# Performance work log

Hardware: AMD Instinct MI355X
Metric: run time of the kernel (lower is better)

The kernel has to match this reference:

```python
import jax, jax.numpy as jnp
import numpy as np

N_NODES = 100000
N_EDGES = 1600000
N_GRAPHS = 512
BN_EPS = 1e-5


def setup_inputs() -> dict:
    key = jax.random.key(0)
    ks = jax.random.split(key, 16)
    x = jax.random.normal(ks[0], (N_NODES, 66), dtype=jnp.float32)
    edge_index = jax.random.randint(ks[1], (2, N_EDGES), 0, N_NODES, dtype=jnp.int64)
    edge_attr = jax.random.normal(ks[2], (N_EDGES, 1), dtype=jnp.float32)
    batch = jnp.sort(jax.random.randint(ks[3], (N_NODES,), 0, N_GRAPHS, dtype=jnp.int64))
    def glorot(k, shape):
        lim = np.sqrt(6.0 / (shape[0] + shape[1]))
        return jax.random.uniform(k, shape, jnp.float32, -lim, lim)
    return {
        "x": x, "edge_index": edge_index, "edge_attr": edge_attr, "batch": batch,
        "W1": glorot(ks[4], (66, 64)), "b1": jnp.zeros((64,), jnp.float32),
        "g1": jnp.ones((64,), jnp.float32), "be1": jnp.zeros((64,), jnp.float32),
        "W2": glorot(ks[5], (64, 32)), "b2": jnp.zeros((32,), jnp.float32),
        "g2": jnp.ones((32,), jnp.float32), "be2": jnp.zeros((32,), jnp.float32),
        "Wm1": glorot(ks[6], (64, 32)), "bm1": jnp.zeros((32,), jnp.float32),
        "Wm2": glorot(ks[7], (32, 2)), "bm2": jnp.zeros((2,), jnp.float32),
    }


def gcn_conv(x, W, b, src, dst, n_nodes):
    # PyG GCNConv: add self-loops, symmetric D^-1/2 (A+I) D^-1/2 normalization.
    xw = x @ W                                             # [N, F]
    deg = jnp.zeros((n_nodes,), xw.dtype).at[dst].add(1.0) + 1.0  # incl. self-loop
    dinv = jax.lax.rsqrt(deg)                              # deg^-1/2
    coef = dinv[src] * dinv[dst]                           # [E]
    agg = jnp.zeros_like(xw).at[dst].add(xw[src] * coef[:, None])
    agg = agg + xw * (dinv * dinv)[:, None]                # self-loop messages
    return agg + b


def batch_norm(x, gamma, beta):
    # training-mode BN over the node dimension (reference is deterministic)
    mu = jnp.mean(x, axis=0)
    var = jnp.mean(jnp.square(x - mu), axis=0)
    return gamma * (x - mu) * jax.lax.rsqrt(var + BN_EPS) + beta


def reference(x, edge_index, edge_attr, batch,
              W1, b1, g1, be1, W2, b2, g2, be2, Wm1, bm1, Wm2, bm2):
    src, dst = edge_index[0], edge_index[1]
    h = x[:, :66]
    h = jax.nn.elu(batch_norm(gcn_conv(h, W1, b1, src, dst, N_NODES), g1, be1))
    # dropout omitted (eval-mode reference)
    h = jax.nn.elu(batch_norm(gcn_conv(h, W2, b2, src, dst, N_NODES), g2, be2))
    counts = jax.ops.segment_sum(jnp.ones((N_NODES,), h.dtype), batch, num_segments=N_GRAPHS)
    mean_pool = jax.ops.segment_sum(h, batch, num_segments=N_GRAPHS) / jnp.maximum(counts, 1.0)[:, None]
    max_pool = jax.ops.segment_max(h, batch, num_segments=N_GRAPHS)
    max_pool = jnp.where(counts[:, None] > 0, max_pool, 0.0)
    g = jnp.concatenate([mean_pool, max_pool], axis=1)     # [G, 64]
    g = jax.nn.elu(g @ Wm1 + bm1)
    return g @ Wm2 + bm2                                   # [G, num_classes]
```

## Files before the change

### kernel.cpp

```cpp
#include <hip/hip_runtime.h>
#include <math.h>

constexpr int NN = 100000;
constexpr int NE = 1600000;
constexpr int NG = 512;
constexpr int NBKT = (NN + 127) / 128;
constexpr int BSTR = 2560;
constexpr int PADREG = BSTR + 896;
constexpr int BCAP = 3072;
constexpr int NHALF = 50048;

typedef unsigned short bf16_t;
typedef unsigned int u32x4 __attribute__((ext_vector_type(4)));
__device__ __forceinline__ bf16_t f2bf(float f) {
    unsigned u = __float_as_uint(f);
    unsigned r = (u + 0x7fffu + ((u >> 16) & 1u)) >> 16;
    return (bf16_t)r;
}
__device__ __forceinline__ float bflo(unsigned u) { return __uint_as_float(u << 16); }
__device__ __forceinline__ float bfhi(unsigned u) { return __uint_as_float(u & 0xffff0000u); }
__device__ __forceinline__ unsigned bfpack(float lo, float hi) {
    return ((unsigned)f2bf(hi) << 16) | (unsigned)f2bf(lo);
}
__device__ __forceinline__ float eluf(float x) {
    return x > 0.f ? x : expm1f(x);
}

__global__ __launch_bounds__(1024) void k_scatter_bkt(const int* __restrict__ src,
                                                      const int* __restrict__ dst,
                                                      int* __restrict__ bktCur,
                                                      int* __restrict__ ebuf) {
    __shared__ int cnt[NBKT];
    __shared__ int base[NBKT];
    int tid = threadIdx.x;
    for (int i = tid; i < NBKT; i += 1024) cnt[i] = 0;
    __syncthreads();
    int per = (NE + gridDim.x - 1) / gridDim.x;
    int e0 = blockIdx.x * per;
    int e1 = min(e0 + per, NE);
    for (int e = e0 + tid; e < e1; e += 1024) {
        int d = __builtin_nontemporal_load(dst + e);
        atomicAdd(&cnt[d >> 7], 1);
    }
    __syncthreads();
    for (int i = tid; i < NBKT; i += 1024) {
        int c = cnt[i];
        base[i] = i * BSTR + (c ? atomicAdd(&bktCur[i], c) : 0);
        cnt[i] = 0;
    }
    __syncthreads();
    for (int e = e0 + tid; e < e1; e += 1024) {
        int s = __builtin_nontemporal_load(src + e);
        int d = __builtin_nontemporal_load(dst + e);
        int b = d >> 7;
        int off = atomicAdd(&cnt[b], 1);
        ebuf[base[b] + off] = (s << 7) | (d & 127);
    }
}

__global__ __launch_bounds__(256) void k_bktsort(const int* __restrict__ bktCur,
                                                 const int* __restrict__ ebuf,
                                                 int* __restrict__ csr,
                                                 int2* __restrict__ rowInfo,
                                                 float* __restrict__ dinv,
                                                 const int* __restrict__ batch,
                                                 int* __restrict__ gptr) {
    int b = blockIdx.x, tid = threadIdx.x;
    if (b == NBKT) {
        for (int g = tid; g <= NG; g += 256) {
            if (g == NG) { gptr[NG] = NN; continue; }
            int lo = 0, hi = NN;
            while (lo < hi) {
                int mid = (lo + hi) >> 1;
                if (batch[mid] < g) lo = mid + 1; else hi = mid;
            }
            gptr[g] = lo;
        }
        return;
    }
    __shared__ int sbuf[BCAP];
    __shared__ int cnt[128], scn[128], cur[128];
    __shared__ int padTotS;
    int base = b * BSTR;
    int n = min(bktCur[b], BSTR);
    int pbase = b * PADREG;
    for (int i = tid; i < n; i += 256) sbuf[i] = __builtin_nontemporal_load(ebuf + base + i);
    if (tid < 128) cnt[tid] = 0;
    __syncthreads();
    for (int i = tid; i < n; i += 256) atomicAdd(&cnt[sbuf[i] & 127], 1);
    __syncthreads();
    int deg = (tid < 128) ? cnt[tid] : 0;
    int pcnt = (deg + 7) & ~7;
    if (tid < 128) scn[tid] = pcnt;
    __syncthreads();
    for (int off = 1; off < 128; off <<= 1) {
        int t = (tid < 128 && tid >= off) ? scn[tid - off] : 0;
        __syncthreads();
        if (tid < 128) scn[tid] += t;
        __syncthreads();
    }
    if (tid == 127) padTotS = scn[127];
    if (tid < 128) {
        int ex = scn[tid] - pcnt;
        cur[tid] = ex;
        int node = b * 128 + tid;
        if (node < NN) {
            rowInfo[node] = make_int2(pbase + ex, pbase + ex + pcnt);
            dinv[node] = rsqrtf((float)deg + 1.0f);
        }
    }
    __syncthreads();
    int padTot = padTotS;
    for (int i = tid; i < padTot; i += 256) csr[pbase + i] = NN;
    __syncthreads();
    for (int i = tid; i < n; i += 256) {
        int p = sbuf[i];
        int pos = atomicAdd(&cur[p & 127], 1);
        csr[pbase + pos] = p >> 7;
    }
}

__global__ void k_gemm1(const float* __restrict__ x, const float* __restrict__ W1,
                        const float* __restrict__ dinv, bf16_t* __restrict__ y1b) {
    __shared__ __align__(16) float sx[64 * 68];
    __shared__ __align__(16) float sw[66 * 64];
    int tid = threadIdx.x;
    for (int i = tid; i < 66 * 32; i += 256) ((float2*)sw)[i] = ((const float2*)W1)[i];
    int base = blockIdx.x * 64;
    int rows = min(64, NN - base);
    int cnt2v = rows * 33;
    const float2* xp = (const float2*)(x + base * 66);
    for (int i = tid; i < cnt2v; i += 256) {
        int r = i / 33, kk = i - r * 33;
        ((float2*)(sx + r * 68))[kk] = xp[i];
    }
    __syncthreads();
    int tr = tid >> 4, tc = tid & 15;
    const float* sxr = sx + tr * 4 * 68;
    const float* swc = sw + tc * 4;
    float acc[4][4];
#pragma unroll
    for (int r = 0; r < 4; ++r)
#pragma unroll
        for (int c = 0; c < 4; ++c) acc[r][c] = 0.f;
#pragma unroll 4
    for (int ks = 0; ks < 64; ks += 4) {
        float4 a0 = *(const float4*)(sxr + 0 * 68 + ks);
        float4 a1 = *(const float4*)(sxr + 1 * 68 + ks);
        float4 a2 = *(const float4*)(sxr + 2 * 68 + ks);
        float4 a3 = *(const float4*)(sxr + 3 * 68 + ks);
        float4 b0 = *(const float4*)(swc + (ks + 0) * 64);
        float4 b1 = *(const float4*)(swc + (ks + 1) * 64);
        float4 b2 = *(const float4*)(swc + (ks + 2) * 64);
        float4 b3 = *(const float4*)(swc + (ks + 3) * 64);
#define FMA4(ar, bv, kk) do { \
        acc[0][0] = fmaf(a0.ar, bv.x, acc[0][0]); acc[0][1] = fmaf(a0.ar, bv.y, acc[0][1]); \
        acc[0][2] = fmaf(a0.ar, bv.z, acc[0][2]); acc[0][3] = fmaf(a0.ar, bv.w, acc[0][3]); \
        acc[1][0] = fmaf(a1.ar, bv.x, acc[1][0]); acc[1][1] = fmaf(a1.ar, bv.y, acc[1][1]); \
        acc[1][2] = fmaf(a1.ar, bv.z, acc[1][2]); acc[1][3] = fmaf(a1.ar, bv.w, acc[1][3]); \
        acc[2][0] = fmaf(a2.ar, bv.x, acc[2][0]); acc[2][1] = fmaf(a2.ar, bv.y, acc[2][1]); \
        acc[2][2] = fmaf(a2.ar, bv.z, acc[2][2]); acc[2][3] = fmaf(a2.ar, bv.w, acc[2][3]); \
        acc[3][0] = fmaf(a3.ar, bv.x, acc[3][0]); acc[3][1] = fmaf(a3.ar, bv.y, acc[3][1]); \
        acc[3][2] = fmaf(a3.ar, bv.z, acc[3][2]); acc[3][3] = fmaf(a3.ar, bv.w, acc[3][3]); } while (0)
        FMA4(x, b0, 0); FMA4(y, b1, 1); FMA4(z, b2, 2); FMA4(w, b3, 3);
#undef FMA4
    }
#pragma unroll
    for (int k = 64; k < 66; ++k) {
        float4 bt = *(const float4*)(swc + k * 64);
#pragma unroll
        for (int r = 0; r < 4; ++r) {
            float av = sxr[r * 68 + k];
            acc[r][0] = fmaf(av, bt.x, acc[r][0]);
            acc[r][1] = fmaf(av, bt.y, acc[r][1]);
            acc[r][2] = fmaf(av, bt.z, acc[r][2]);
            acc[r][3] = fmaf(av, bt.w, acc[r][3]);
        }
    }
    bf16_t* dstp = y1b + (tc >> 2) * ((NN + 1) * 16) + (tc & 3) * 4;
#pragma unroll
    for (int r = 0; r < 4; ++r) {
        int nn = base + tr * 4 + r;
        if (nn < NN) {
            float di = dinv[nn];
            ushort4 o;
            o.x = f2bf(di * acc[r][0]); o.y = f2bf(di * acc[r][1]);
            o.z = f2bf(di * acc[r][2]); o.w = f2bf(di * acc[r][3]);
            *(ushort4*)(dstp + (size_t)nn * 16) = o;
        } else if (nn == NN) {
            ushort4 o; o.x = 0; o.y = 0; o.z = 0; o.w = 0;
            *(ushort4*)(dstp + (size_t)nn * 16) = o;
        }
    }
}

template<int NSL>
__global__ __launch_bounds__(256) void k_gather(const int2* __restrict__ rowInfo,
                                                const int* __restrict__ csr,
                                                const float* __restrict__ dinv,
                                                const uint4* __restrict__ yb,
                                                uint4* __restrict__ aggb,
                                                float* __restrict__ sums,
                                                float* __restrict__ sqs,
                                                int n0, int n1) {
    constexpr int SH = (NSL == 4) ? 2 : 1;
    __shared__ float sSum[16], sSq[16];
    int tid = threadIdx.x;
    if (tid < 16) { sSum[tid] = 0.f; sSq[tid] = 0.f; }
    __syncthreads();
    int slice = blockIdx.x & (NSL - 1);
    int part = blockIdx.x >> SH;
    int nparts = gridDim.x >> SH;
    int lane = tid & 1;
    int grp = tid >> 1;
    const uint4* y = yb + (size_t)slice * ((NN + 1) * 2) + lane;
    uint4* agg = aggb + (size_t)slice * (NN * 2) + lane;
    float s[8], q[8];
#pragma unroll
    for (int k = 0; k < 8; ++k) { s[k] = 0.f; q[k] = 0.f; }
    for (int n = n0 + part * 128 + grp; n < n1; n += nparts * 128) {
        int2 ri = rowInfo[n];
        float a[8];
#pragma unroll
        for (int k = 0; k < 8; ++k) a[k] = 0.f;
        int j = ri.x;
        unsigned long long c0 = 0, c1 = 0, c2 = 0, c3 = 0;
        if (j < ri.y) {
            const unsigned long long* cp = (const unsigned long long*)(csr + j);
            c0 = cp[0]; c1 = cp[1]; c2 = cp[2]; c3 = cp[3];
        }
        while (j < ri.y) {
            int i0 = (int)(c0 & 0xffffffffu), i1 = (int)(c0 >> 32);
            int i2 = (int)(c1 & 0xffffffffu), i3 = (int)(c1 >> 32);
            int i4 = (int)(c2 & 0xffffffffu), i5 = (int)(c2 >> 32);
            int i6 = (int)(c3 & 0xffffffffu), i7 = (int)(c3 >> 32);
            j += 8;
            uint4 v0 = y[i0 * 2];
            uint4 v1 = y[i1 * 2];
            uint4 v2 = y[i2 * 2];
            uint4 v3 = y[i3 * 2];
            uint4 v4 = y[i4 * 2];
            uint4 v5 = y[i5 * 2];
            uint4 v6 = y[i6 * 2];
            uint4 v7 = y[i7 * 2];
            if (j < ri.y) {
                const unsigned long long* np = (const unsigned long long*)(csr + j);
                c0 = np[0]; c1 = np[1]; c2 = np[2]; c3 = np[3];
            }
#define ACC8(v) do { \
            a[0] += bflo((v).x); a[1] += bfhi((v).x); \
            a[2] += bflo((v).y); a[3] += bfhi((v).y); \
            a[4] += bflo((v).z); a[5] += bfhi((v).z); \
            a[6] += bflo((v).w); a[7] += bfhi((v).w); } while (0)
            ACC8(v0); ACC8(v1); ACC8(v2); ACC8(v3);
            ACC8(v4); ACC8(v5); ACC8(v6); ACC8(v7);
#undef ACC8
        }
        uint4 vs = y[n * 2];
        float di = dinv[n];
        a[0] = di * (a[0] + bflo(vs.x)); a[1] = di * (a[1] + bfhi(vs.x));
        a[2] = di * (a[2] + bflo(vs.y)); a[3] = di * (a[3] + bfhi(vs.y));
        a[4] = di * (a[4] + bflo(vs.z)); a[5] = di * (a[5] + bfhi(vs.z));
        a[6] = di * (a[6] + bflo(vs.w)); a[7] = di * (a[7] + bfhi(vs.w));
        u32x4 o;
        o.x = bfpack(a[0], a[1]); o.y = bfpack(a[2], a[3]);
        o.z = bfpack(a[4], a[5]); o.w = bfpack(a[6], a[7]);
        __builtin_nontemporal_store(o, (u32x4*)(agg + n * 2));
#pragma unroll
        for (int k = 0; k < 8; ++k) {
            float av = (k == 0) ? a[0] : (k == 1) ? a[1] : (k == 2) ? a[2] : (k == 3) ? a[3]
                     : (k == 4) ? a[4] : (k == 5) ? a[5] : (k == 6) ? a[6] : a[7];
            s[k] += av; q[k] += av * av;
        }
    }
#pragma unroll
    for (int k = 0; k < 8; ++k) {
        float sv = s[k], qv = q[k];
#pragma unroll
        for (int off = 2; off < 64; off <<= 1) {
            sv += __shfl_xor(sv, off);
            qv += __shfl_xor(qv, off);
        }
        if ((tid & 63) < 2) {
            atomicAdd(&sSum[lane * 8 + k], sv);
            atomicAdd(&sSq[lane * 8 + k], qv);
        }
    }
    __syncthreads();
    if (tid < 16) {
        unsafeAtomicAdd(&sums[slice * 16 + tid], sSum[tid]);
        unsafeAtomicAdd(&sqs[slice * 16 + tid], sSq[tid]);
    }
}

__global__ void k_bn_gemm2(const unsigned* __restrict__ agg1b, const float* __restrict__ sums,
                           const float* __restrict__ sqs, const float* __restrict__ gamma,
                           const float* __restrict__ beta, const float* __restrict__ W2,
                           const float* __restrict__ dinv, bf16_t* __restrict__ y2b) {
    constexpr int RB = 32;
    __shared__ __align__(16) float sh[RB * 64];
    __shared__ __align__(16) float sWt[32 * 68];
    __shared__ float sscale[64], sshift[64];
    int tid = threadIdx.x;
    if (tid < 64) {
        float mu = sums[tid] * (1.0f / NN);
        float var = sqs[tid] * (1.0f / NN) - mu * mu;
        float sc = gamma[tid] * rsqrtf(var + 1e-5f);
        sscale[tid] = sc;
        sshift[tid] = beta[tid] - mu * sc;
    }
#pragma unroll
    for (int i = tid; i < 64 * 32; i += 256) {
        int k = i >> 5, c = i & 31;
        sWt[c * 68 + k] = W2[i];
    }
    __syncthreads();
    int base = blockIdx.x * RB;
#pragma unroll
    for (int rr = 0; rr < RB / 8; ++rr) {
        int r = (tid >> 5) + rr * 8, qq = tid & 31;
        int slice = qq >> 3, lane = qq & 7;
        int n = base + r;
        int col = slice * 16 + lane * 2;
        float v0 = 0.f, v1 = 0.f;
        if (n < NN) {
            unsigned u = agg1b[(size_t)slice * NN * 8 + (size_t)n * 8 + lane];
            v0 = eluf(fmaf(bflo(u), sscale[col], sshift[col]));
            v1 = eluf(fmaf(bfhi(u), sscale[col + 1], sshift[col + 1]));
        }
        sh[r * 64 + col] = v0;
        sh[r * 64 + col + 1] = v1;
    }
    __syncthreads();
    int c = tid & 31;
    bf16_t* dstp = y2b + (c >> 4) * ((NN + 1) * 16) + (c & 15);
    const float* swr = sWt + c * 68;
#pragma unroll
    for (int rr = 0; rr < RB / 8; ++rr) {
        int r = (tid >> 5) + rr * 8;
        int n = base + r;
        if (n < NN) {
            const float* shr = sh + r * 64;
            float acc = 0.f;
#pragma unroll
            for (int k4 = 0; k4 < 64; k4 += 4) {
                float4 av = *(const float4*)(shr + k4);
                float4 bv = *(const float4*)(swr + k4);
                acc = fmaf(av.x, bv.x, acc);
                acc = fmaf(av.y, bv.y, acc);
                acc = fmaf(av.z, bv.z, acc);
                acc = fmaf(av.w, bv.w, acc);
            }
            dstp[(size_t)n * 16] = f2bf(dinv[n] * acc);
        } else if (n == NN) {
            dstp[(size_t)NN * 16] = 0;
        }
    }
}

__global__ void k_poolmlp(const unsigned* __restrict__ agg2b, const float* __restrict__ sums,
                          const float* __restrict__ sqs, const float* __restrict__ gamma,
                          const float* __restrict__ beta, const int* __restrict__ gptr,
                          const float* __restrict__ Wm1, const float* __restrict__ bm1,
                          const float* __restrict__ Wm2, const float* __restrict__ bm2,
                          float* __restrict__ out) {
    __shared__ float sscale[32], sshift[32];
    __shared__ float red[256];
    __shared__ float gr[64];
    __shared__ float h[32];
    int tid = threadIdx.x;
    if (tid < 32) {
        float mu = sums[tid] * (1.0f / NN);
        float var = sqs[tid] * (1.0f / NN) - mu * mu;
        float sc = gamma[tid] * rsqrtf(var + 1e-5f);
        sscale[tid] = sc;
        sshift[tid] = beta[tid] - mu * sc;
    }
    __syncthreads();
    int g = blockIdx.x;
    int c = tid & 31, r = tid >> 5;
    int beg = gptr[g], end = gptr[g + 1];
    float scl = sscale[c], shf = sshift[c];
    const unsigned* ap = agg2b + (size_t)(c >> 4) * NN * 8 + ((c >> 1) & 7);
    bool hi = (c & 1);
    float s = 0.f, m = -INFINITY;
    for (int n = beg + r; n < end; n += 8) {
        unsigned u = ap[n * 8];
        float v = eluf(fmaf(hi ? bfhi(u) : bflo(u), scl, shf));
        s += v;
        m = fmaxf(m, v);
    }
    red[tid] = s;
    __syncthreads();
    int cnt = end - beg;
    if (r == 0) {
        float stot = 0.f;
#pragma unroll
        for (int i = 0; i < 8; ++i) stot += red[i * 32 + c];
        gr[c] = stot / fmaxf((float)cnt, 1.f);
    }
    __syncthreads();
    red[tid] = m;
    __syncthreads();
    if (r == 0) {
        float mtot = -INFINITY;
#pragma unroll
        for (int i = 0; i < 8; ++i) mtot = fmaxf(mtot, red[i * 32 + c]);
        gr[32 + c] = (cnt > 0) ? mtot : 0.f;
    }
    __syncthreads();
    if (tid < 32) {
        float acc = bm1[tid];
#pragma unroll
        for (int k = 0; k < 64; ++k) acc = fmaf(gr[k], Wm1[k * 32 + tid], acc);
        h[tid] = eluf(acc);
    }
    __syncthreads();
    if (tid < 2) {
        float acc = bm2[tid];
#pragma unroll
        for (int k = 0; k < 32; ++k) acc = fmaf(h[k], Wm2[k * 2 + tid], acc);
        out[g * 2 + tid] = acc;
    }
}

extern "C" void kernel_launch(void* const* d_in, const int* in_sizes, int n_in,
                              void* d_out, int out_size, void* d_ws, size_t ws_size,
                              hipStream_t stream) {
    const float* x    = (const float*)d_in[0];
    const int*   eidx = (const int*)d_in[1];
    const int*   src  = eidx;
    const int*   dst  = eidx + NE;
    const int*   batch = (const int*)d_in[3];
    const float* W1  = (const float*)d_in[4];
    const float* g1  = (const float*)d_in[6];
    const float* be1 = (const float*)d_in[7];
    const float* W2  = (const float*)d_in[8];
    const float* g2  = (const float*)d_in[10];
    const float* be2 = (const float*)d_in[11];
    const float* Wm1 = (const float*)d_in[12];
    const float* bm1 = (const float*)d_in[13];
    const float* Wm2 = (const float*)d_in[14];
    const float* bm2 = (const float*)d_in[15];
    float* out = (float*)d_out;

    constexpr int CSRSZ = NBKT * PADREG + 16;
    int*    bktCur  = (int*)d_ws;
    float*  S       = (float*)(bktCur + 800);
    int*    gptr    = (int*)(S + 512);
    int*    csr     = gptr + 544;
    int2*   rowInfo = (int2*)(csr + CSRSZ);
    float*  dinv    = (float*)(rowInfo + 100000);
    bf16_t* y1b     = (bf16_t*)(dinv + 100000);
    bf16_t* agg1b   = y1b + (NN + 1) * 64;
    bf16_t* y2b     = agg1b + NN * 64;
    bf16_t* agg2b   = y2b + (NN + 1) * 32;
    int*    ebuf    = (int*)y2b;

    float* sum1 = S;        float* sq1 = S + 64;
    float* sum2 = S + 128;  float* sq2 = S + 160;

    (void)hipMemsetAsync(bktCur, 0, (800 + 512) * sizeof(int), stream);

    k_scatter_bkt<<<512, 1024, 0, stream>>>(src, dst, bktCur, ebuf);
    k_bktsort<<<NBKT + 1, 256, 0, stream>>>(bktCur, ebuf, csr, rowInfo, dinv, batch, gptr);

    k_gemm1<<<(NN + 63) / 64, 256, 0, stream>>>(x, W1, dinv, y1b);
    k_gather<4><<<1564, 256, 0, stream>>>(rowInfo, csr, dinv,
                                          (const uint4*)y1b, (uint4*)agg1b,
                                          sum1, sq1, 0, NHALF);
    k_gather<4><<<1564, 256, 0, stream>>>(rowInfo, csr, dinv,
                                          (const uint4*)y1b, (uint4*)agg1b,
                                          sum1, sq1, NHALF, NN);

    k_bn_gemm2<<<NN / 32 + 1, 256, 0, stream>>>((const unsigned*)agg1b, sum1, sq1,
                                                g1, be1, W2, dinv, y2b);
    k_gather<2><<<782, 256, 0, stream>>>(rowInfo, csr, dinv,
                                         (const uint4*)y2b, (uint4*)agg2b,
                                         sum2, sq2, 0, NHALF);
    k_gather<2><<<782, 256, 0, stream>>>(rowInfo, csr, dinv,
                                         (const uint4*)y2b, (uint4*)agg2b,
                                         sum2, sq2, NHALF, NN);

    k_poolmlp<<<NG, 256, 0, stream>>>((const unsigned*)agg2b, sum2, sq2, g2, be2, gptr,
                                      Wm1, bm1, Wm2, bm2, out);
}
```

Baseline: 304.1 us.

## Fuse bucket sort with first GEMM and merge split gather launches

Merges the bucket-sort kernel and the first GEMM into one launch. GEMM blocks compute node degrees locally from the bucketed edge buffer instead of waiting for dinv from the sort kernel. The two half-range gather launches per layer are also merged into single launches with doubled grids. This removes launch gaps and the sort-to-GEMM dependency, at the cost of GEMM blocks rescanning each bucket's edges (twice per bucket) and larger shared memory per block.

New measurement: 280.9 us. -7.6%, faster.

```diff
diff --git a/kernel.cpp b/kernel.cpp
--- a/kernel.cpp
+++ b/kernel.cpp
@@ -8,7 +8,7 @@
 constexpr int BSTR = 2560;
 constexpr int PADREG = BSTR + 896;
 constexpr int BCAP = 3072;
-constexpr int NHALF = 50048;
+constexpr int NT1 = (NN + 63) / 64;
 
 typedef unsigned short bf16_t;
 typedef unsigned int u32x4 __attribute__((ext_vector_type(4)));
@@ -58,14 +58,101 @@
     }
 }
 
-__global__ __launch_bounds__(256) void k_bktsort(const int* __restrict__ bktCur,
-                                                 const int* __restrict__ ebuf,
-                                                 int* __restrict__ csr,
-                                                 int2* __restrict__ rowInfo,
-                                                 float* __restrict__ dinv,
-                                                 const int* __restrict__ batch,
-                                                 int* __restrict__ gptr) {
-    int b = blockIdx.x, tid = threadIdx.x;
+__global__ __launch_bounds__(256) void k_sort_gemm1(const int* __restrict__ bktCur,
+                                                    const int* __restrict__ ebuf,
+                                                    int* __restrict__ csr,
+                                                    int2* __restrict__ rowInfo,
+                                                    float* __restrict__ dinv,
+                                                    const int* __restrict__ batch,
+                                                    int* __restrict__ gptr,
+                                                    const float* __restrict__ x,
+                                                    const float* __restrict__ W1,
+                                                    bf16_t* __restrict__ y1b) {
+    __shared__ __align__(16) unsigned smem_u[8640];
+    int tid = threadIdx.x;
+    if (blockIdx.x < NT1) {
+        float* sx = (float*)smem_u;
+        float* sw = sx + 64 * 68;
+        int*  deg = (int*)(sw + 66 * 64);
+        if (tid < 64) deg[tid] = 0;
+        for (int i = tid; i < 66 * 32; i += 256) ((float2*)sw)[i] = ((const float2*)W1)[i];
+        int base = blockIdx.x * 64;
+        int rows = min(64, NN - base);
+        int cnt2v = rows * 33;
+        const float2* xp = (const float2*)(x + base * 66);
+        for (int i = tid; i < cnt2v; i += 256) {
+            int r = i / 33, kk = i - r * 33;
+            ((float2*)(sx + r * 68))[kk] = xp[i];
+        }
+        int bkt = base >> 7;
+        int half = (base >> 6) & 1;
+        int ne = min(bktCur[bkt], BSTR);
+        for (int i = tid; i < ne; i += 256) {
+            int e = ebuf[bkt * BSTR + i];
+            int d = e & 127;
+            if ((d >> 6) == half) atomicAdd(&deg[d & 63], 1);
+        }
+        __syncthreads();
+        int tr = tid >> 4, tc = tid & 15;
+        const float* sxr = sx + tr * 4 * 68;
+        const float* swc = sw + tc * 4;
+        float acc[4][4];
+#pragma unroll
+        for (int r = 0; r < 4; ++r)
+#pragma unroll
+            for (int c = 0; c < 4; ++c) acc[r][c] = 0.f;
+#pragma unroll 4
+        for (int ks = 0; ks < 64; ks += 4) {
+            float4 a0 = *(const float4*)(sxr + 0 * 68 + ks);
+            float4 a1 = *(const float4*)(sxr + 1 * 68 + ks);
+            float4 a2 = *(const float4*)(sxr + 2 * 68 + ks);
+            float4 a3 = *(const float4*)(sxr + 3 * 68 + ks);
+            float4 b0 = *(const float4*)(swc + (ks + 0) * 64);
+            float4 b1 = *(const float4*)(swc + (ks + 1) * 64);
+            float4 b2 = *(const float4*)(swc + (ks + 2) * 64);
+            float4 b3 = *(const float4*)(swc + (ks + 3) * 64);
+#define FMA4(ar, bv) do { \
+            acc[0][0] = fmaf(a0.ar, bv.x, acc[0][0]); acc[0][1] = fmaf(a0.ar, bv.y, acc[0][1]); \
+            acc[0][2] = fmaf(a0.ar, bv.z, acc[0][2]); acc[0][3] = fmaf(a0.ar, bv.w, acc[0][3]); \
+            acc[1][0] = fmaf(a1.ar, bv.x, acc[1][0]); acc[1][1] = fmaf(a1.ar, bv.y, acc[1][1]); \
+            acc[1][2] = fmaf(a1.ar, bv.z, acc[1][2]); acc[1][3] = fmaf(a1.ar, bv.w, acc[1][3]); \
+            acc[2][0] = fmaf(a2.ar, bv.x, acc[2][0]); acc[2][1] = fmaf(a2.ar, bv.y, acc[2][1]); \
+            acc[2][2] = fmaf(a2.ar, bv.z, acc[2][2]); acc[2][3] = fmaf(a2.ar, bv.w, acc[2][3]); \
+            acc[3][0] = fmaf(a3.ar, bv.x, acc[3][0]); acc[3][1] = fmaf(a3.ar, bv.y, acc[3][1]); \
+            acc[3][2] = fmaf(a3.ar, bv.z, acc[3][2]); acc[3][3] = fmaf(a3.ar, bv.w, acc[3][3]); } while (0)
+            FMA4(x, b0); FMA4(y, b1); FMA4(z, b2); FMA4(w, b3);
+#undef FMA4
+        }
+#pragma unroll
+        for (int k = 64; k < 66; ++k) {
+            float4 bt = *(const float4*)(swc + k * 64);
+#pragma unroll
+            for (int r = 0; r < 4; ++r) {
+                float av = sxr[r * 68 + k];
+                acc[r][0] = fmaf(av, bt.x, acc[r][0]);
+                acc[r][1] = fmaf(av, bt.y, acc[r][1]);
+                acc[r][2] = fmaf(av, bt.z, acc[r][2]);
+                acc[r][3] = fmaf(av, bt.w, acc[r][3]);
+            }
+        }
+        bf16_t* dstp = y1b + (tc >> 2) * ((NN + 1) * 16) + (tc & 3) * 4;
+#pragma unroll
+        for (int r = 0; r < 4; ++r) {
+            int nn = base + tr * 4 + r;
+            if (nn < NN) {
+                float di = rsqrtf((float)deg[tr * 4 + r] + 1.0f);
+                ushort4 o;
+                o.x = f2bf(di * acc[r][0]); o.y = f2bf(di * acc[r][1]);
+                o.z = f2bf(di * acc[r][2]); o.w = f2bf(di * acc[r][3]);
+                *(ushort4*)(dstp + (size_t)nn * 16) = o;
+            } else if (nn == NN) {
+                ushort4 o; o.x = 0; o.y = 0; o.z = 0; o.w = 0;
+                *(ushort4*)(dstp + (size_t)nn * 16) = o;
+            }
+        }
+        return;
+    }
+    int b = blockIdx.x - NT1;
     if (b == NBKT) {
         for (int g = tid; g <= NG; g += 256) {
             if (g == NG) { gptr[NG] = NN; continue; }
@@ -78,9 +165,11 @@
         }
         return;
     }
-    __shared__ int sbuf[BCAP];
-    __shared__ int cnt[128], scn[128], cur[128];
-    __shared__ int padTotS;
+    int* sbuf = (int*)smem_u;
+    int* cnt  = sbuf + BCAP;
+    int* scn  = cnt + 128;
+    int* cur  = scn + 128;
+    int* padTotS = cur + 128;
     int base = b * BSTR;
     int n = min(bktCur[b], BSTR);
     int pbase = b * PADREG;
@@ -99,7 +188,7 @@
         if (tid < 128) scn[tid] += t;
         __syncthreads();
     }
-    if (tid == 127) padTotS = scn[127];
+    if (tid == 127) *padTotS = scn[127];
     if (tid < 128) {
         int ex = scn[tid] - pcnt;
         cur[tid] = ex;
@@ -110,87 +199,13 @@
         }
     }
     __syncthreads();
-    int padTot = padTotS;
+    int padTot = *padTotS;
     for (int i = tid; i < padTot; i += 256) csr[pbase + i] = NN;
     __syncthreads();
     for (int i = tid; i < n; i += 256) {
         int p = sbuf[i];
         int pos = atomicAdd(&cur[p & 127], 1);
         csr[pbase + pos] = p >> 7;
-    }
-}
-
-__global__ void k_gemm1(const float* __restrict__ x, const float* __restrict__ W1,
-                        const float* __restrict__ dinv, bf16_t* __restrict__ y1b) {
-    __shared__ __align__(16) float sx[64 * 68];
-    __shared__ __align__(16) float sw[66 * 64];
-    int tid = threadIdx.x;
-    for (int i = tid; i < 66 * 32; i += 256) ((float2*)sw)[i] = ((const float2*)W1)[i];
-    int base = blockIdx.x * 64;
-    int rows = min(64, NN - base);
-    int cnt2v = rows * 33;
-    const float2* xp = (const float2*)(x + base * 66);
-    for (int i = tid; i < cnt2v; i += 256) {
-        int r = i / 33, kk = i - r * 33;
-        ((float2*)(sx + r * 68))[kk] = xp[i];
-    }
-    __syncthreads();
-    int tr = tid >> 4, tc = tid & 15;
-    const float* sxr = sx + tr * 4 * 68;
-    const float* swc = sw + tc * 4;
-    float acc[4][4];
-#pragma unroll
-    for (int r = 0; r < 4; ++r)
-#pragma unroll
-        for (int c = 0; c < 4; ++c) acc[r][c] = 0.f;
-#pragma unroll 4
-    for (int ks = 0; ks < 64; ks += 4) {
-        float4 a0 = *(const float4*)(sxr + 0 * 68 + ks);
-        float4 a1 = *(const float4*)(sxr + 1 * 68 + ks);
-        float4 a2 = *(const float4*)(sxr + 2 * 68 + ks);
-        float4 a3 = *(const float4*)(sxr + 3 * 68 + ks);
-        float4 b0 = *(const float4*)(swc + (ks + 0) * 64);
-        float4 b1 = *(const float4*)(swc + (ks + 1) * 64);
-        float4 b2 = *(const float4*)(swc + (ks + 2) * 64);
-        float4 b3 = *(const float4*)(swc + (ks + 3) * 64);
-#define FMA4(ar, bv, kk) do { \
-        acc[0][0] = fmaf(a0.ar, bv.x, acc[0][0]); acc[0][1] = fmaf(a0.ar, bv.y, acc[0][1]); \
-        acc[0][2] = fmaf(a0.ar, bv.z, acc[0][2]); acc[0][3] = fmaf(a0.ar, bv.w, acc[0][3]); \
-        acc[1][0] = fmaf(a1.ar, bv.x, acc[1][0]); acc[1][1] = fmaf(a1.ar, bv.y, acc[1][1]); \
-        acc[1][2] = fmaf(a1.ar, bv.z, acc[1][2]); acc[1][3] = fmaf(a1.ar, bv.w, acc[1][3]); \
-        acc[2][0] = fmaf(a2.ar, bv.x, acc[2][0]); acc[2][1] = fmaf(a2.ar, bv.y, acc[2][1]); \
-        acc[2][2] = fmaf(a2.ar, bv.z, acc[2][2]); acc[2][3] = fmaf(a2.ar, bv.w, acc[2][3]); \
-        acc[3][0] = fmaf(a3.ar, bv.x, acc[3][0]); acc[3][1] = fmaf(a3.ar, bv.y, acc[3][1]); \
-        acc[3][2] = fmaf(a3.ar, bv.z, acc[3][2]); acc[3][3] = fmaf(a3.ar, bv.w, acc[3][3]); } while (0)
-        FMA4(x, b0, 0); FMA4(y, b1, 1); FMA4(z, b2, 2); FMA4(w, b3, 3);
-#undef FMA4
-    }
-#pragma unroll
-    for (int k = 64; k < 66; ++k) {
-        float4 bt = *(const float4*)(swc + k * 64);
-#pragma unroll
-        for (int r = 0; r < 4; ++r) {
-            float av = sxr[r * 68 + k];
-            acc[r][0] = fmaf(av, bt.x, acc[r][0]);
-            acc[r][1] = fmaf(av, bt.y, acc[r][1]);
-            acc[r][2] = fmaf(av, bt.z, acc[r][2]);
-            acc[r][3] = fmaf(av, bt.w, acc[r][3]);
-        }
-    }
-    bf16_t* dstp = y1b + (tc >> 2) * ((NN + 1) * 16) + (tc & 3) * 4;
-#pragma unroll
-    for (int r = 0; r < 4; ++r) {
-        int nn = base + tr * 4 + r;
-        if (nn < NN) {
-            float di = dinv[nn];
-            ushort4 o;
-            o.x = f2bf(di * acc[r][0]); o.y = f2bf(di * acc[r][1]);
-            o.z = f2bf(di * acc[r][2]); o.w = f2bf(di * acc[r][3]);
-            *(ushort4*)(dstp + (size_t)nn * 16) = o;
-        } else if (nn == NN) {
-            ushort4 o; o.x = 0; o.y = 0; o.z = 0; o.w = 0;
-            *(ushort4*)(dstp + (size_t)nn * 16) = o;
-        }
     }
 }
 
@@ -201,8 +216,7 @@
                                                 const uint4* __restrict__ yb,
                                                 uint4* __restrict__ aggb,
                                                 float* __restrict__ sums,
-                                                float* __restrict__ sqs,
-                                                int n0, int n1) {
+                                                float* __restrict__ sqs) {
     constexpr int SH = (NSL == 4) ? 2 : 1;
     __shared__ float sSum[16], sSq[16];
     int tid = threadIdx.x;
@@ -218,7 +232,7 @@
     float s[8], q[8];
 #pragma unroll
     for (int k = 0; k < 8; ++k) { s[k] = 0.f; q[k] = 0.f; }
-    for (int n = n0 + part * 128 + grp; n < n1; n += nparts * 128) {
+    for (int n = part * 128 + grp; n < NN; n += nparts * 128) {
         int2 ri = rowInfo[n];
         float a[8];
 #pragma unroll
@@ -463,24 +477,18 @@
     (void)hipMemsetAsync(bktCur, 0, (800 + 512) * sizeof(int), stream);
 
     k_scatter_bkt<<<512, 1024, 0, stream>>>(src, dst, bktCur, ebuf);
-    k_bktsort<<<NBKT + 1, 256, 0, stream>>>(bktCur, ebuf, csr, rowInfo, dinv, batch, gptr);
-
-    k_gemm1<<<(NN + 63) / 64, 256, 0, stream>>>(x, W1, dinv, y1b);
-    k_gather<4><<<1564, 256, 0, stream>>>(rowInfo, csr, dinv,
+    k_sort_gemm1<<<NT1 + NBKT + 1, 256, 0, stream>>>(bktCur, ebuf, csr, rowInfo, dinv,
+                                                     batch, gptr, x, W1, y1b);
+
+    k_gather<4><<<3128, 256, 0, stream>>>(rowInfo, csr, dinv,
                                           (const uint4*)y1b, (uint4*)agg1b,
-                                          sum1, sq1, 0, NHALF);
-    k_gather<4><<<1564, 256, 0, stream>>>(rowInfo, csr, dinv,
-                                          (const uint4*)y1b, (uint4*)agg1b,
-                                          sum1, sq1, NHALF, NN);
+                                          sum1, sq1);
 
     k_bn_gemm2<<<NN / 32 + 1, 256, 0, stream>>>((const unsigned*)agg1b, sum1, sq1,
                                                 g1, be1, W2, dinv, y2b);
-    k_gather<2><<<782, 256, 0, stream>>>(rowInfo, csr, dinv,
-                                         (const uint4*)y2b, (uint4*)agg2b,
-                                         sum2, sq2, 0, NHALF);
-    k_gather<2><<<782, 256, 0, stream>>>(rowInfo, csr, dinv,
-                                         (const uint4*)y2b, (uint4*)agg2b,
-                                         sum2, sq2, NHALF, NN);
+    k_gather<2><<<1564, 256, 0, stream>>>(rowInfo, csr, dinv,
+                                          (const uint4*)y2b, (uint4*)agg2b,
+                                          sum2, sq2);
 
     k_poolmlp<<<NG, 256, 0, stream>>>((const unsigned*)agg2b, sum2, sq2, g2, be2, gptr,
                                       Wm1, bm1, Wm2, bm2, out);
```
